# Optimization experiments

Hardware: AMD Instinct MI355X
Metric: run time of the kernel (lower is better)

Reference implementation:

```python
import jax, jax.numpy as jnp
import numpy as np

B, S, HID, NH, HD, NL = 2, 4096, 1024, 16, 64, 128
N_ITER = 6


def setup_inputs() -> dict:
    key = jax.random.key(0)
    ks = jax.random.split(key, 9)
    s = 0.02
    D = NH * HD
    return {
        "X": jax.random.normal(ks[0], (B, S, HID), jnp.float32),
        "mask": jnp.ones((B, S), jnp.float32),
        "Wq": jax.random.normal(ks[1], (HID, D), jnp.float32) * s,
        "bq": jnp.zeros((D,), jnp.float32),
        "Wk": jax.random.normal(ks[2], (HID, D), jnp.float32) * s,
        "bk": jnp.zeros((D,), jnp.float32),
        "Wv": jax.random.normal(ks[3], (HID, D), jnp.float32) * s,
        "bv": jnp.zeros((D,), jnp.float32),
        "Wo": jax.random.normal(ks[4], (D, HID), jnp.float32) * s,
        "bo": jnp.zeros((HID,), jnp.float32),
    }


def iterative_inv(mat, n_iter=N_ITER):
    # Newton-Schulz style pseudo-inverse iteration (Nystromformer 'original' init)
    I = jnp.eye(mat.shape[-1], dtype=mat.dtype)
    K = mat
    V = K.swapaxes(-1, -2) / jnp.max(jnp.sum(K, axis=-2))
    for _ in range(n_iter):
        KV = K @ V
        V = 0.25 * V @ (13.0 * I - KV @ (15.0 * I - KV @ (7.0 * I - KV)))
    return V


def nystrom_core(Q, K, V, mask):
    # Q,K,V: [B,NH,S,HD], mask: [B,S]
    scale = 1.0 / np.sqrt(np.sqrt(HD))  # 1/d^(1/4) applied to both Q and K
    m = mask[:, None, :, None]
    Q = Q * m * scale
    K = K * m * scale
    seg = S // NL
    # landmarks: mean over contiguous segments -> [B,NH,NL,HD]
    Ql = Q.reshape(B, NH, NL, seg, HD).mean(axis=-2)
    Kl = K.reshape(B, NH, NL, seg, HD).mean(axis=-2)
    k1 = jax.nn.softmax(jnp.einsum('bhsd,bhld->bhsl', Q, Kl), axis=-1)   # [B,NH,S,NL]
    k2 = jax.nn.softmax(jnp.einsum('bhld,bhmd->bhlm', Ql, Kl), axis=-1)  # [B,NH,NL,NL]
    k3 = jax.nn.softmax(
        jnp.einsum('bhld,bhsd->bhls', Ql, K) - 1e9 * (1.0 - mask[:, None, None, :]),
        axis=-1)                                                          # [B,NH,NL,S]
    return k1 @ iterative_inv(k2) @ (k3 @ V)                              # [B,NH,S,HD]


def reference(X, mask, Wq, bq, Wk, bk, Wv, bv, Wo, bo):
    def split(Y):  # [B,S,NH*HD] -> [B,NH,S,HD]
        return Y.reshape(B, S, NH, HD).transpose(0, 2, 1, 3)
    Q = split(X @ Wq + bq)
    K = split(X @ Wk + bk)
    V = split(X @ Wv + bv)
    attn = nystrom_core(Q.astype(jnp.float32), K.astype(jnp.float32),
                        V.astype(jnp.float32), mask.astype(jnp.float32))
    out = attn.transpose(0, 2, 1, 3).reshape(B, S, NH * HD)
    return out @ Wo + bo
```

## Files before the change

kernel.cpp:

```cpp
#include <hip/hip_runtime.h>
#include <math.h>

constexpr int cB = 2, cS = 4096, cHID = 1024, cNH = 16, cHD = 64, cNL = 128, cSEG = 32, cD = 1024, cBH = 32;
constexpr float cSCALE = 0.35355339059327373f;

typedef _Float16 f16x8 __attribute__((ext_vector_type(8)));
typedef float f32x4 __attribute__((ext_vector_type(4)));

__device__ inline void gload_lds16(const void* g, void* l) {
    __builtin_amdgcn_global_load_lds(
        (const __attribute__((address_space(1))) void*)g,
        (__attribute__((address_space(3))) void*)l, 16, 0, 0);
}

__global__ __launch_bounds__(256) void wcast_t(
    const float* __restrict__ Wq, const float* __restrict__ Wk,
    const float* __restrict__ Wv, const float* __restrict__ Wo,
    _Float16* __restrict__ WqT, _Float16* __restrict__ WkT,
    _Float16* __restrict__ WvT, _Float16* __restrict__ WoT)
{
    __shared__ float tile[32][33];
    const int wsel = blockIdx.z;
    const float* W = (wsel == 0) ? Wq : (wsel == 1 ? Wk : (wsel == 2 ? Wv : Wo));
    _Float16* WT   = (wsel == 0) ? WqT : (wsel == 1 ? WkT : (wsel == 2 ? WvT : WoT));
    const int n0 = blockIdx.x * 32, k0 = blockIdx.y * 32;
    const int t = threadIdx.x;
    const int r = t >> 3, c = (t & 7) * 4;
    float4 v = *reinterpret_cast<const float4*>(W + (size_t)(k0 + r) * cD + n0 + c);
    tile[r][c] = v.x; tile[r][c + 1] = v.y; tile[r][c + 2] = v.z; tile[r][c + 3] = v.w;
    __syncthreads();
    union { _Float16 h[4]; ushort4 u; } p;
    p.h[0] = (_Float16)tile[c + 0][r]; p.h[1] = (_Float16)tile[c + 1][r];
    p.h[2] = (_Float16)tile[c + 2][r]; p.h[3] = (_Float16)tile[c + 3][r];
    *reinterpret_cast<ushort4*>(WT + (size_t)(n0 + r) * cHID + k0 + c) = p.u;
}

__global__ __launch_bounds__(256) void xm_kernel(
    const float* __restrict__ X, const float* __restrict__ mask,
    float* __restrict__ Xm, float* __restrict__ mbar, _Float16* __restrict__ Xh)
{
    const int bl = blockIdx.x;
    const int b = bl >> 7, l = bl & 127;
    const int c = threadIdx.x * 4;
    float4 a = {0.f, 0.f, 0.f, 0.f};
    float msum = 0.f;
    for (int j = 0; j < cSEG; ++j) {
        float m = mask[b * cS + l * cSEG + j];
        size_t roff = ((size_t)(b * cS + l * cSEG + j)) * cHID + c;
        float4 x = *reinterpret_cast<const float4*>(X + roff);
        union { _Float16 h[4]; ushort4 u; } p;
        p.h[0] = (_Float16)x.x; p.h[1] = (_Float16)x.y;
        p.h[2] = (_Float16)x.z; p.h[3] = (_Float16)x.w;
        *reinterpret_cast<ushort4*>(Xh + roff) = p.u;
        a.x += m * x.x; a.y += m * x.y; a.z += m * x.z; a.w += m * x.w;
        msum += m;
    }
    const float inv = 1.0f / cSEG;
    a.x *= inv; a.y *= inv; a.z *= inv; a.w *= inv;
    *reinterpret_cast<float4*>(Xm + (size_t)bl * cHID + c) = a;
    if (threadIdx.x == 0) mbar[bl] = msum * inv;
}

__global__ __launch_bounds__(256) void qkv_gemm_f16(
    const _Float16* __restrict__ Xh, const float* __restrict__ mask,
    const _Float16* __restrict__ WqT, const _Float16* __restrict__ WkT, const _Float16* __restrict__ WvT,
    const float* __restrict__ bq, const float* __restrict__ bk, const float* __restrict__ bv,
    _Float16* __restrict__ Qh, _Float16* __restrict__ Kh, _Float16* __restrict__ Vh)
{
    __shared__ __align__(16) _Float16 As[128 * 64];
    __shared__ __align__(16) _Float16 Bs[128 * 64];
    const int wsel = blockIdx.z;
    const _Float16* WT = (wsel == 0) ? WqT : (wsel == 1 ? WkT : WvT);
    const float* bias  = (wsel == 0) ? bq  : (wsel == 1 ? bk  : bv);
    _Float16* Y        = (wsel == 0) ? Qh  : (wsel == 1 ? Kh  : Vh);
    const int orig = blockIdx.x;
    const int xcd = orig & 7, idx = orig >> 3;
    const int n0 = (idx & 7) * 128;
    const int m0 = (xcd * 8 + (idx >> 3)) * 128;
    const int t = threadIdx.x;
    const int wave = t >> 6, lane = t & 63;
    const int wm = (wave >> 1) * 64, wn = (wave & 1) * 64;
    const int quad = lane >> 4, l15 = lane & 15;
    const int srow = wave * 8 + (lane >> 3);
    const int scol = ((lane & 7) ^ (lane >> 3)) * 8;

    f32x4 acc[4][4];
#pragma unroll
    for (int i = 0; i < 4; ++i)
#pragma unroll
        for (int j = 0; j < 4; ++j) acc[i][j] = (f32x4){0.f, 0.f, 0.f, 0.f};

    for (int k0 = 0; k0 < cHID; k0 += 64) {
        const _Float16* aSrc = Xh + (size_t)(m0 + srow) * cHID + k0 + scol;
// ... 216 lines not shown
        for (int mt_ = 0; mt_ < 4; ++mt_) {                                             \
            const int rowL_ = wr * 64 + mt_ * 16 + l15;                                 \
            _Pragma("unroll")                                                           \
            for (int k0_ = 0; k0_ < 4; ++k0_) {                                         \
                LH[mt_][k0_] = *reinterpret_cast<const f16x8*>(&PH[rowL_ * 136 + k0_ * 32 + quad * 8]); \
                LL[mt_][k0_] = *reinterpret_cast<const f16x8*>(&PL[rowL_ * 136 + k0_ * 32 + quad * 8]); \
            }                                                                           \
        }                                                                               \
    }

#define NYS_PRODUCT(PH, PL, LH, LL)                                                     \
    {                                                                                   \
        _Pragma("unroll")                                                               \
        for (int mt_ = 0; mt_ < 4; ++mt_)                                               \
            _Pragma("unroll")                                                           \
            for (int nt_ = 0; nt_ < 2; ++nt_) acc[mt_][nt_] = (f32x4){0.f, 0.f, 0.f, 0.f}; \
        _Pragma("unroll")                                                               \
        for (int nt_ = 0; nt_ < 2; ++nt_) {                                             \
            _Pragma("unroll")                                                           \
            for (int k0_ = 0; k0_ < 4; ++k0_) {                                         \
                const int boff_ = (wcb + nt_ * 16) * 136 + k0_ * 32 + quad * 8;         \
                f16x8 bh_ = *reinterpret_cast<const f16x8*>(&PH[boff_]);                \
                f16x8 bl_ = *reinterpret_cast<const f16x8*>(&PL[boff_]);                \
                _Pragma("unroll")                                                       \
                for (int mt_ = 0; mt_ < 4; ++mt_) {                                     \
                    acc[mt_][nt_] = NYS_MFMA(LH[mt_][k0_], bh_, acc[mt_][nt_]);         \
                    acc[mt_][nt_] = NYS_MFMA(LL[mt_][k0_], bh_, acc[mt_][nt_]);         \
                    acc[mt_][nt_] = NYS_MFMA(LH[mt_][k0_], bl_, acc[mt_][nt_]);         \
                }                                                                       \
            }                                                                           \
        }                                                                               \
    }

__global__ __launch_bounds__(512, 2) void nys_fused(
    const float* __restrict__ k2, const int* __restrict__ cmax,
    float* __restrict__ Mg0, float* __restrict__ Mg1)
{
    __shared__ __align__(16) _Float16 Ahi_s[128 * 136];
    __shared__ __align__(16) _Float16 Alo_s[128 * 136];
    __shared__ __align__(16) _Float16 Whi_s[128 * 136];
    __shared__ __align__(16) _Float16 Wlo_s[128 * 136];
    const int bh = blockIdx.x;
    const int t = threadIdx.x;
    const int wave = t >> 6, lane = t & 63;
    const int wr = wave >> 2, wc = wave & 3;
    const int quad = lane >> 4, l15 = lane & 15;
    const int wcb = wc * 32 + l15;
    const float* Kg = k2 + (size_t)bh * 16384;
    float* Mg0b = Mg0 + (size_t)bh * 16384;
    float* Mg1b = Mg1 + (size_t)bh * 16384;
    const float sc = sqrtf(1.0f / __int_as_float(*cmax));

    {
        const int row = t >> 2, c0 = (t & 3) * 32;
        const float* src = Kg + row * 128 + c0;
        _Float16* dh = &Whi_s[row * 136 + c0];
        _Float16* dl = &Wlo_s[row * 136 + c0];
#pragma unroll
        for (int u = 0; u < 32; u += 4) {
            float4 v = *reinterpret_cast<const float4*>(src + u);
            ushort4 ph, pl; _Float16 h, l;
            split2(v.x * sc, h, l); ph.x = f16bits(h); pl.x = f16bits(l);
            split2(v.y * sc, h, l); ph.y = f16bits(h); pl.y = f16bits(l);
            split2(v.z * sc, h, l); ph.z = f16bits(h); pl.z = f16bits(l);
            split2(v.w * sc, h, l); ph.w = f16bits(h); pl.w = f16bits(l);
            *reinterpret_cast<ushort4*>(dh + u) = ph;
            *reinterpret_cast<ushort4*>(dl + u) = pl;
        }
    }
    __syncthreads();

    f32x4 acc[4][2];
    f16x8 Fh[4][4], Fl[4][4];

    NYS_PRELOAD(Whi_s, Wlo_s, Fh, Fl);
    NYS_PRODUCT(Whi_s, Wlo_s, Fh, Fl);
#pragma unroll
    for (int mt = 0; mt < 4; ++mt)
#pragma unroll
        for (int nt = 0; nt < 2; ++nt) {
            const int col = wcb + nt * 16;
            const int rb  = wr * 64 + mt * 16 + quad * 4;
            ushort4 ph, pl;
#pragma unroll
            for (int r = 0; r < 4; ++r) {
                _Float16 h, l; split2(acc[mt][nt][r], h, l);
                ((unsigned short*)&ph)[r] = f16bits(h);
                ((unsigned short*)&pl)[r] = f16bits(l);
            }
            *reinterpret_cast<ushort4*>(&Ahi_s[col * 136 + rb]) = ph;
            *reinterpret_cast<ushort4*>(&Alo_s[col * 136 + rb]) = pl;
        }
    __syncthreads();

    for (int it = 0; it < 6; ++it) {
        NYS_PRELOAD(Ahi_s, Alo_s, Fh, Fl);
        NYS_PRODUCT(Ahi_s, Alo_s, Fh, Fl);
#pragma unroll
        for (int mt = 0; mt < 4; ++mt)
#pragma unroll
            for (int nt = 0; nt < 2; ++nt) {
                const int col = wcb + nt * 16;
                const int rb  = wr * 64 + mt * 16 + quad * 4;
                ushort4 ah = *reinterpret_cast<const ushort4*>(&Ahi_s[col * 136 + rb]);
                ushort4 al = *reinterpret_cast<const ushort4*>(&Alo_s[col * 136 + rb]);
                ushort4 ph, pl;
#pragma unroll
                for (int r = 0; r < 4; ++r) {
                    float av = (float)__builtin_bit_cast(_Float16, ((unsigned short*)&ah)[r])
                             + (float)__builtin_bit_cast(_Float16, ((unsigned short*)&al)[r]);
                    float v = ((rb + r) == col ? 15.0f : 0.0f) - 7.0f * av + acc[mt][nt][r];
                    _Float16 h, l; split2(v, h, l);
                    ((unsigned short*)&ph)[r] = f16bits(h);
                    ((unsigned short*)&pl)[r] = f16bits(l);
                }
                *reinterpret_cast<ushort4*>(&Whi_s[col * 136 + rb]) = ph;
                *reinterpret_cast<ushort4*>(&Wlo_s[col * 136 + rb]) = pl;
            }
        __syncthreads();
        NYS_PRODUCT(Whi_s, Wlo_s, Fh, Fl);
        __syncthreads();
#pragma unroll
        for (int mt = 0; mt < 4; ++mt)
#pragma unroll
            for (int nt = 0; nt < 2; ++nt) {
                const int col = wcb + nt * 16;
                const int rb  = wr * 64 + mt * 16 + quad * 4;
                ushort4 ph, pl; float4 mv;
#pragma unroll
                for (int r = 0; r < 4; ++r) {
                    float v = ((rb + r) == col ? 13.0f : 0.0f) - acc[mt][nt][r];
                    _Float16 h, l; split2(v, h, l);
                    ((unsigned short*)&ph)[r] = f16bits(h);
                    ((unsigned short*)&pl)[r] = f16bits(l);
                    ((float*)&mv)[r] = 0.25f * v;
                }
                *reinterpret_cast<ushort4*>(&Whi_s[col * 136 + rb]) = ph;
                *reinterpret_cast<ushort4*>(&Wlo_s[col * 136 + rb]) = pl;
                if (it == 0)
                    *reinterpret_cast<float4*>(&Mg0b[col * 128 + rb]) = mv;
            }
        __syncthreads();
        NYS_PRODUCT(Whi_s, Wlo_s, Fh, Fl);
#pragma unroll
        for (int mt = 0; mt < 4; ++mt)
#pragma unroll
            for (int nt = 0; nt < 2; ++nt) {
                const int col = wcb + nt * 16;
                const int rb  = wr * 64 + mt * 16 + quad * 4;
                ushort4 ph, pl;
#pragma unroll
                for (int r = 0; r < 4; ++r) {
                    _Float16 h, l; split2(0.25f * acc[mt][nt][r], h, l);
                    ((unsigned short*)&ph)[r] = f16bits(h);
                    ((unsigned short*)&pl)[r] = f16bits(l);
                }
                *reinterpret_cast<ushort4*>(&Ahi_s[col * 136 + rb]) = ph;
                *reinterpret_cast<ushort4*>(&Alo_s[col * 136 + rb]) = pl;
            }
        if (it >= 1) {
            const float* Mr = (it & 1) ? Mg0b : Mg1b;
            float*       Mw = (it & 1) ? Mg1b : Mg0b;
#pragma unroll
            for (int mt = 0; mt < 4; ++mt)
#pragma unroll
                for (int nt = 0; nt < 2; ++nt) acc[mt][nt] = (f32x4){0.f, 0.f, 0.f, 0.f};
#pragma unroll
            for (int k0 = 0; k0 < 4; ++k0) {
                f16x8 Mh[4], Ml[4];
#pragma unroll
                for (int mt = 0; mt < 4; ++mt) {
                    const int rowL = wr * 64 + mt * 16 + l15;
                    const float* src = Mr + rowL * 128 + k0 * 32 + quad * 8;
                    float4 v0 = *reinterpret_cast<const float4*>(src);
                    float4 v1 = *reinterpret_cast<const float4*>(src + 4);
                    union { f16x8 v; _Float16 e[8]; } hh, ll;
                    split2(v0.x, hh.e[0], ll.e[0]); split2(v0.y, hh.e[1], ll.e[1]);
                    split2(v0.z, hh.e[2], ll.e[2]); split2(v0.w, hh.e[3], ll.e[3]);
                    split2(v1.x, hh.e[4], ll.e[4]); split2(v1.y, hh.e[5], ll.e[5]);
                    split2(v1.z, hh.e[6], ll.e[6]); split2(v1.w, hh.e[7], ll.e[7]);
                    Mh[mt] = hh.v; Ml[mt] = ll.v;
                }
#pragma unroll
                for (int nt = 0; nt < 2; ++nt) {
                    const int boff = (wcb + nt * 16) * 136 + k0 * 32 + quad * 8;
                    f16x8 bh_ = *reinterpret_cast<const f16x8*>(&Whi_s[boff]);
                    f16x8 bl_ = *reinterpret_cast<const f16x8*>(&Wlo_s[boff]);
#pragma unroll
                    for (int mt = 0; mt < 4; ++mt) {
                        acc[mt][nt] = NYS_MFMA(Mh[mt], bh_, acc[mt][nt]);
                        acc[mt][nt] = NYS_MFMA(Ml[mt], bh_, acc[mt][nt]);
                        acc[mt][nt] = NYS_MFMA(Mh[mt], bl_, acc[mt][nt]);
                    }
                }
            }
#pragma unroll
            for (int mt = 0; mt < 4; ++mt)
#pragma unroll
                for (int nt = 0; nt < 2; ++nt) {
                    const int col = wcb + nt * 16;
                    const int rb  = wr * 64 + mt * 16 + quad * 4;
                    float4 mv;
#pragma unroll
                    for (int r = 0; r < 4; ++r) ((float*)&mv)[r] = 0.25f * acc[mt][nt][r];
                    *reinterpret_cast<float4*>(&Mw[col * 128 + rb]) = mv;
                }
        }
        __syncthreads();
    }
}

__global__ __launch_bounds__(256) void vtrans(const _Float16* __restrict__ Vh, _Float16* __restrict__ VTh)
{
    __shared__ ushort T[64][72];
    const int s0 = blockIdx.x * 64, bh = blockIdx.y;
    const int t = threadIdx.x;
    const _Float16* vb = Vh + ((size_t)bh * cS + s0) * cHD;
#pragma unroll
    for (int i = 0; i < 2; ++i) {
        int idx = t + i * 256;
        int row = idx >> 3, c8 = idx & 7;
        f16x8 v = *reinterpret_cast<const f16x8*>(vb + (size_t)row * cHD + c8 * 8);
#pragma unroll
        for (int j = 0; j < 8; ++j) T[row][c8 * 8 + j] = ((ushort*)&v)[j];
    }
    __syncthreads();
    _Float16* vt = VTh + (size_t)bh * cHD * cS;
#pragma unroll
    for (int i = 0; i < 2; ++i) {
        int idx = t + i * 256;
        int d = idx >> 3, s8 = idx & 7;
        f16x8 o;
#pragma unroll
        for (int j = 0; j < 8; ++j) ((ushort*)&o)[j] = T[s8 * 8 + j][d];
        *reinterpret_cast<f16x8*>(vt + (size_t)d * cS + s0 + s8 * 8) = o;
    }
}

__global__ __launch_bounds__(256) void k3v_mfma(
    const _Float16* __restrict__ Qlh, const _Float16* __restrict__ Kh,
    const _Float16* __restrict__ VTh, const float* __restrict__ mask,
    float* __restrict__ Opart, float* __restrict__ mpart, float* __restrict__ spart)
{
    __shared__ __align__(16) _Float16 Ps[128 * 72];
    __shared__ float msk[256];
    const int z = blockIdx.x, bh = blockIdx.y;
    const int b = bh >> 4;
    const int sbase = z * 256;
    const int t = threadIdx.x;
    const int wave = t >> 6, lane = t & 63;
    const int quad = lane >> 4, l15 = lane & 15;

    msk[t] = mask[b * cS + sbase + t];

    f16x8 aq[2][2];
    const _Float16* qlg = Qlh + (size_t)bh * cNL * cHD;
#pragma unroll
    for (int mt = 0; mt < 2; ++mt)
#pragma unroll
        for (int k0 = 0; k0 < 2; ++k0)
            aq[mt][k0] = *reinterpret_cast<const f16x8*>(
                qlg + (size_t)(wave * 32 + mt * 16 + l15) * cHD + k0 * 32 + quad * 8);

    float mrun[2][4], srun[2][4];
    f32x4 accO[2][4];
#pragma unroll
    for (int mt = 0; mt < 2; ++mt)
#pragma unroll
        for (int r = 0; r < 4; ++r) { mrun[mt][r] = -1e30f; srun[mt][r] = 0.f; }
#pragma unroll
    for (int mt = 0; mt < 2; ++mt)
#pragma unroll
        for (int dt = 0; dt < 4; ++dt) accO[mt][dt] = (f32x4){0.f, 0.f, 0.f, 0.f};

    __syncthreads();

    const _Float16* kg = Kh + (size_t)bh * cS * cHD;
    const _Float16* vg = VTh + (size_t)bh * cHD * cS;

    for (int step = 0; step < 4; ++step) {
        const int st = sbase + step * 64;
        f32x4 accS[2][4];
#pragma unroll
        for (int mt = 0; mt < 2; ++mt)
#pragma unroll
            for (int nt = 0; nt < 4; ++nt) accS[mt][nt] = (f32x4){0.f, 0.f, 0.f, 0.f};
#pragma unroll
        for (int k0 = 0; k0 < 2; ++k0)
#pragma unroll
            for (int nt = 0; nt < 4; ++nt) {
                f16x8 bk = *reinterpret_cast<const f16x8*>(
                    kg + (size_t)(st + nt * 16 + l15) * cHD + k0 * 32 + quad * 8);
#pragma unroll
                for (int mt = 0; mt < 2; ++mt)
                    accS[mt][nt] = __builtin_amdgcn_mfma_f32_16x16x32_f16(aq[mt][k0], bk, accS[mt][nt], 0, 0, 0);
            }
#pragma unroll
        for (int nt = 0; nt < 4; ++nt) {
            float pen = 1e9f * (1.0f - msk[step * 64 + nt * 16 + l15]);
#pragma unroll
            for (int mt = 0; mt < 2; ++mt)
#pragma unroll
                for (int r = 0; r < 4; ++r) accS[mt][nt][r] -= pen;
        }
#pragma unroll
        for (int mt = 0; mt < 2; ++mt) {
#pragma unroll
            for (int r = 0; r < 4; ++r) {
                float tmax = fmaxf(fmaxf(accS[mt][0][r], accS[mt][1][r]),
                                   fmaxf(accS[mt][2][r], accS[mt][3][r]));
#pragma unroll
                for (int w = 1; w < 16; w <<= 1) tmax = fmaxf(tmax, __shfl_xor(tmax, w, 16));
                float mnew = fmaxf(mrun[mt][r], tmax);
                float alpha = __expf(mrun[mt][r] - mnew);
                float ts = 0.f;
#pragma unroll
                for (int nt = 0; nt < 4; ++nt) {
                    float e = __expf(accS[mt][nt][r] - mnew);
                    accS[mt][nt][r] = e; ts += e;
                }
#pragma unroll
                for (int w = 1; w < 16; w <<= 1) ts += __shfl_xor(ts, w, 16);
                srun[mt][r] = srun[mt][r] * alpha + ts;
                mrun[mt][r] = mnew;
#pragma unroll
                for (int dt = 0; dt < 4; ++dt) accO[mt][dt][r] *= alpha;
            }
        }
#pragma unroll
        for (int mt = 0; mt < 2; ++mt)
#pragma unroll
            for (int nt = 0; nt < 4; ++nt)
#pragma unroll
                for (int r = 0; r < 4; ++r)
                    Ps[(wave * 32 + mt * 16 + quad * 4 + r) * 72 + nt * 16 + l15] =
                        (_Float16)accS[mt][nt][r];
#pragma unroll
        for (int k0 = 0; k0 < 2; ++k0) {
            f16x8 ap[2];
#pragma unroll
            for (int mt = 0; mt < 2; ++mt)
                ap[mt] = *reinterpret_cast<const f16x8*>(
                    &Ps[(wave * 32 + mt * 16 + l15) * 72 + k0 * 32 + quad * 8]);
#pragma unroll
            for (int dt = 0; dt < 4; ++dt) {
                f16x8 bv = *reinterpret_cast<const f16x8*>(
                    vg + (size_t)(dt * 16 + l15) * cS + st + k0 * 32 + quad * 8);
#pragma unroll
                for (int mt = 0; mt < 2; ++mt)
                    accO[mt][dt] = __builtin_amdgcn_mfma_f32_16x16x32_f16(ap[mt], bv, accO[mt][dt], 0, 0, 0);
            }
        }
    }
    const int rowbase = bh * cNL + wave * 32;
#pragma unroll
    for (int mt = 0; mt < 2; ++mt)
#pragma unroll
        for (int dt = 0; dt < 4; ++dt)
#pragma unroll
            for (int r = 0; r < 4; ++r)
                Opart[(size_t)(z * 4096 + rowbase + mt * 16 + quad * 4 + r) * cHD + dt * 16 + l15] =
                    accO[mt][dt][r];
    if (l15 == 0) {
#pragma unroll
        for (int mt = 0; mt < 2; ++mt)
#pragma unroll
            for (int r = 0; r < 4; ++r) {
                int prow = z * 4096 + rowbase + mt * 16 + quad * 4 + r;
                mpart[prow] = mrun[mt][r];
                spart[prow] = srun[mt][r];
            }
    }
}

__global__ __launch_bounds__(256) void k3v_reduce(
    const float* __restrict__ Opart, const float* __restrict__ mpart,
    const float* __restrict__ spart, float* __restrict__ CV)
{
    const int t = threadIdx.x;
    const int row = blockIdx.x * 4 + (t >> 6);
    const int d = t & 63;
    float mstar = -1e30f;
#pragma unroll
    for (int z = 0; z < 16; ++z) mstar = fmaxf(mstar, mpart[z * 4096 + row]);
    float ssum = 0.f, acc = 0.f;
#pragma unroll
    for (int z = 0; z < 16; ++z) {
        float w = __expf(mpart[z * 4096 + row] - mstar);
        ssum += w * spart[z * 4096 + row];
        acc  += w * Opart[(size_t)(z * 4096 + row) * cHD + d];
    }
    CV[(size_t)row * cHD + d] = acc / ssum;
}

__global__ __launch_bounds__(256) void w2_matmul(
    const float* __restrict__ k2, const float* __restrict__ M6,
    const int* __restrict__ cmax, const float* __restrict__ CV,
    _Float16* __restrict__ W2T)
{
    __shared__ __align__(16) float CVs[128][68];
    __shared__ __align__(16) float Us[128][68];
    const int bh = blockIdx.x, t = threadIdx.x;
    const float invc = 1.0f / __int_as_float(*cmax);
    for (int k = 0; k < 32; ++k) { int idx = t + k * 256; CVs[idx >> 6][idx & 63] = CV[(size_t)bh * 8192 + idx]; }
    __syncthreads();
    const float* Mg = M6 + (size_t)bh * 16384;
    {
        const int tx = t & 15, ty = t >> 4;
        float acc[8][4] = {};
        for (int k = 0; k < 128; ++k) {
            float4 b4 = *reinterpret_cast<const float4*>(&CVs[k][tx * 4]);
#pragma unroll
            for (int i = 0; i < 8; ++i) {
                float a = Mg[(ty * 8 + i) * 128 + k];
                acc[i][0] += a * b4.x; acc[i][1] += a * b4.y; acc[i][2] += a * b4.z; acc[i][3] += a * b4.w;
            }
        }
#pragma unroll
        for (int i = 0; i < 8; ++i)
#pragma unroll
            for (int j = 0; j < 4; ++j)
                Us[ty * 8 + i][tx * 4 + j] = acc[i][j];
    }
    __syncthreads();
    {
        const int l = t & 127, dg = (t >> 7) * 32;
        float acc2[32];
#pragma unroll
        for (int dd = 0; dd < 32; ++dd) acc2[dd] = 0.f;
        const float* kg = k2 + (size_t)bh * 16384;
        for (int j = 0; j < 128; ++j) {
            float kv = kg[j * 128 + l];
#pragma unroll
            for (int dd = 0; dd < 32; ++dd) acc2[dd] += kv * Us[j][dg + dd];
        }
        _Float16* wt = W2T + (size_t)bh * (cHD * cNL);
#pragma unroll
// ... 96 lines not shown
{
    const float* X    = (const float*)d_in[0];
    const float* mask = (const float*)d_in[1];
    const float* Wq   = (const float*)d_in[2];
    const float* bq   = (const float*)d_in[3];
    const float* Wk   = (const float*)d_in[4];
    const float* bk   = (const float*)d_in[5];
    const float* Wv   = (const float*)d_in[6];
    const float* bv   = (const float*)d_in[7];
    const float* Wo   = (const float*)d_in[8];
    const float* bo   = (const float*)d_in[9];
    float* out = (float*)d_out;

    float* ws = (float*)d_ws;
    size_t off = 0;
    const size_t szQKV = (size_t)cBH * cS * cHD;
    const size_t szL   = (size_t)cBH * cNL * cHD;
    const size_t szM   = (size_t)cBH * cNL * cNL;
    float* Qr   = ws + off; off += szQKV;
    float* Kr   = ws + off; off += szQKV;
    float* Vr   = ws + off; off += szQKV;
    _Float16* Xh  = (_Float16*)(ws + off); off += szQKV / 2;
    _Float16* WqT = (_Float16*)(ws + off); off += 524288;
    _Float16* WkT = (_Float16*)(ws + off); off += 524288;
    _Float16* WvT = (_Float16*)(ws + off); off += 524288;
    _Float16* WoT = (_Float16*)(ws + off); off += 524288;
    float* Xm   = ws + off; off += (size_t)cB * cNL * cHID;
    float* mbar = ws + off; off += 256;
    float* Ql  = ws + off; off += szL;
    float* Kl  = ws + off; off += szL;
    float* k2  = ws + off; off += szM;
    float* Mg0 = ws + off; off += szM;
    float* Mg1 = ws + off; off += szM;
    float* Zb  = ws + off; off += szM;
    float* T2b = ws + off; off += szM;
    float* T3b = ws + off; off += szM;
    float* CV  = ws + off; off += szL;
    _Float16* Qlh  = (_Float16*)(ws + off); off += szL / 2;
    _Float16* Klh  = (_Float16*)(ws + off); off += szL / 2;
    _Float16* W2Th = (_Float16*)(ws + off); off += szL / 2;
    int*   cmax = (int*)(ws + off); off += 16;
    float* mpart = ws + off; off += 65536;
    float* spart = ws + off; off += 65536;

    _Float16* Qh   = (_Float16*)Qr;
    float*    Opart = Qr + szQKV / 2;
    _Float16* Kh   = (_Float16*)Kr;
    _Float16* ctxh = (_Float16*)(Kr + szQKV / 2);
    _Float16* Vh   = (_Float16*)Vr;
    _Float16* VTh  = (_Float16*)(Vr + szQKV / 2);

    (void)Zb; (void)T2b; (void)T3b;

    hipMemsetAsync(cmax, 0, sizeof(int), stream);

    wcast_t<<<dim3(32, 32, 4), 256, 0, stream>>>(Wq, Wk, Wv, Wo, WqT, WkT, WvT, WoT);
    xm_kernel<<<cB * cNL, 256, 0, stream>>>(X, mask, Xm, mbar, Xh);

    qkv_gemm_f16<<<dim3(512, 1, 3), 256, 0, stream>>>(
        Xh, mask, WqT, WkT, WvT, bq, bk, bv, Qh, Kh, Vh);
    vtrans<<<dim3(cS / 64, cBH), 256, 0, stream>>>(Vh, VTh);
    lgemm<<<dim3(cD / 64, (cB * cNL) / 64, 2), 256, 0, stream>>>(Xm, mbar, Wq, bq, Wk, bk, Ql, Kl, Qlh, Klh);

    k2_softmax<<<cBH * cNL, 128, 0, stream>>>(Ql, Kl, k2);
    colsum_max<<<cBH, 128, 0, stream>>>(k2, cmax);

    nys_fused<<<cBH, 512, 0, stream>>>(k2, cmax, Mg0, Mg1);

    k3v_mfma<<<dim3(16, cBH), 256, 0, stream>>>(Qlh, Kh, VTh, mask, Opart, mpart, spart);
    k3v_reduce<<<1024, 256, 0, stream>>>(Opart, mpart, spart, CV);
    w2_matmul<<<cBH, 256, 0, stream>>>(k2, Mg1, cmax, CV, W2Th);
    k1_mfma<<<dim3(cS / 64, cBH), 256, 0, stream>>>(Qh, Klh, W2Th, ctxh);
    out_gemm_f16<<<dim3(512), 256, 0, stream>>>(ctxh, WoT, bo, out);
}
```

Measured before the change: 474.2 us.

## Co-schedule Newton-Schulz inverse with k3·V in one launch, fold reduce into w2

The 32-block serial Newton-Schulz inverse kernel and the k3·V flash-style partial kernel now run as a single launch. The first 32 blocks do the inverse and the remaining 256 blocks each run two k3v work-groups of 4 waves, so the two independent stages overlap on the GPU. The k3v_reduce kernel is removed and its log-sum-exp combine is done inside w2_matmul when it loads CV. xm_kernel is split across 4 blocks of 64 threads per segment to raise parallelism. The cost is that the heterogeneous blocks share one large LDS allocation sized for the inverse path, which may limit occupancy for the k3v blocks, and w2_matmul now repeats redundant reduction work.

Measured after the change: 476.5 us. About the same (+0.5%).

```diff
diff --git a/kernel.cpp b/kernel.cpp
--- a/kernel.cpp
+++ b/kernel.cpp
@@ -35,13 +35,14 @@
     *reinterpret_cast<ushort4*>(WT + (size_t)(n0 + r) * cHID + k0 + c) = p.u;
 }
 
-__global__ __launch_bounds__(256) void xm_kernel(
+__global__ __launch_bounds__(64) void xm_kernel(
     const float* __restrict__ X, const float* __restrict__ mask,
     float* __restrict__ Xm, float* __restrict__ mbar, _Float16* __restrict__ Xh)
 {
     const int bl = blockIdx.x;
+    const int q  = blockIdx.y;
     const int b = bl >> 7, l = bl & 127;
-    const int c = threadIdx.x * 4;
+    const int c = q * 256 + threadIdx.x * 4;
     float4 a = {0.f, 0.f, 0.f, 0.f};
     float msum = 0.f;
     for (int j = 0; j < cSEG; ++j) {
@@ -58,7 +59,7 @@
     const float inv = 1.0f / cSEG;
     a.x *= inv; a.y *= inv; a.z *= inv; a.w *= inv;
     *reinterpret_cast<float4*>(Xm + (size_t)bl * cHID + c) = a;
-    if (threadIdx.x == 0) mbar[bl] = msum * inv;
+    if (q == 0 && threadIdx.x == 0) mbar[bl] = msum * inv;
 }
 
 __global__ __launch_bounds__(256) void qkv_gemm_f16(
@@ -341,115 +342,54 @@
         }                                                                               \
     }
 
-__global__ __launch_bounds__(512, 2) void nys_fused(
+__global__ __launch_bounds__(512, 2) void nys_k3v(
     const float* __restrict__ k2, const int* __restrict__ cmax,
-    float* __restrict__ Mg0, float* __restrict__ Mg1)
-{
-    __shared__ __align__(16) _Float16 Ahi_s[128 * 136];
-    __shared__ __align__(16) _Float16 Alo_s[128 * 136];
-    __shared__ __align__(16) _Float16 Whi_s[128 * 136];
-    __shared__ __align__(16) _Float16 Wlo_s[128 * 136];
-    const int bh = blockIdx.x;
-    const int t = threadIdx.x;
-    const int wave = t >> 6, lane = t & 63;
-    const int wr = wave >> 2, wc = wave & 3;
-    const int quad = lane >> 4, l15 = lane & 15;
-    const int wcb = wc * 32 + l15;
-    const float* Kg = k2 + (size_t)bh * 16384;
-    float* Mg0b = Mg0 + (size_t)bh * 16384;
-    float* Mg1b = Mg1 + (size_t)bh * 16384;
-    const float sc = sqrtf(1.0f / __int_as_float(*cmax));
-
-    {
-        const int row = t >> 2, c0 = (t & 3) * 32;
-        const float* src = Kg + row * 128 + c0;
-        _Float16* dh = &Whi_s[row * 136 + c0];
-        _Float16* dl = &Wlo_s[row * 136 + c0];
-#pragma unroll
-        for (int u = 0; u < 32; u += 4) {
-            float4 v = *reinterpret_cast<const float4*>(src + u);
-            ushort4 ph, pl; _Float16 h, l;
-            split2(v.x * sc, h, l); ph.x = f16bits(h); pl.x = f16bits(l);
-            split2(v.y * sc, h, l); ph.y = f16bits(h); pl.y = f16bits(l);
-            split2(v.z * sc, h, l); ph.z = f16bits(h); pl.z = f16bits(l);
-            split2(v.w * sc, h, l); ph.w = f16bits(h); pl.w = f16bits(l);
-            *reinterpret_cast<ushort4*>(dh + u) = ph;
-            *reinterpret_cast<ushort4*>(dl + u) = pl;
-        }
-    }
-    __syncthreads();
-
-    f32x4 acc[4][2];
-    f16x8 Fh[4][4], Fl[4][4];
-
-    NYS_PRELOAD(Whi_s, Wlo_s, Fh, Fl);
-    NYS_PRODUCT(Whi_s, Wlo_s, Fh, Fl);
-#pragma unroll
-    for (int mt = 0; mt < 4; ++mt)
-#pragma unroll
-        for (int nt = 0; nt < 2; ++nt) {
-            const int col = wcb + nt * 16;
-            const int rb  = wr * 64 + mt * 16 + quad * 4;
-            ushort4 ph, pl;
-#pragma unroll
-            for (int r = 0; r < 4; ++r) {
-                _Float16 h, l; split2(acc[mt][nt][r], h, l);
-                ((unsigned short*)&ph)[r] = f16bits(h);
-                ((unsigned short*)&pl)[r] = f16bits(l);
+    float* __restrict__ Mg0, float* __restrict__ Mg1,
+    const _Float16* __restrict__ Qlh, const _Float16* __restrict__ Kh,
+    const _Float16* __restrict__ VTh, const float* __restrict__ mask,
+    float* __restrict__ Opart, float* __restrict__ mpart, float* __restrict__ spart)
+{
+    __shared__ __align__(16) _Float16 SMEM[4 * 128 * 136];
+
+    if (blockIdx.x < 32) {
+        _Float16* Ahi_s = SMEM;
+        _Float16* Alo_s = SMEM + 128 * 136;
+        _Float16* Whi_s = SMEM + 2 * 128 * 136;
+        _Float16* Wlo_s = SMEM + 3 * 128 * 136;
+        const int bh = blockIdx.x;
+        const int t = threadIdx.x;
+        const int wave = t >> 6, lane = t & 63;
+        const int wr = wave >> 2, wc = wave & 3;
+        const int quad = lane >> 4, l15 = lane & 15;
+        const int wcb = wc * 32 + l15;
+        const float* Kg = k2 + (size_t)bh * 16384;
+        float* Mg0b = Mg0 + (size_t)bh * 16384;
+        float* Mg1b = Mg1 + (size_t)bh * 16384;
+        const float sc = sqrtf(1.0f / __int_as_float(*cmax));
+
+        {
+            const int row = t >> 2, c0 = (t & 3) * 32;
+            const float* src = Kg + row * 128 + c0;
+            _Float16* dh = &Whi_s[row * 136 + c0];
+            _Float16* dl = &Wlo_s[row * 136 + c0];
+#pragma unroll
+            for (int u = 0; u < 32; u += 4) {
+                float4 v = *reinterpret_cast<const float4*>(src + u);
+                ushort4 ph, pl; _Float16 h, l;
+                split2(v.x * sc, h, l); ph.x = f16bits(h); pl.x = f16bits(l);
+                split2(v.y * sc, h, l); ph.y = f16bits(h); pl.y = f16bits(l);
+                split2(v.z * sc, h, l); ph.z = f16bits(h); pl.z = f16bits(l);
+                split2(v.w * sc, h, l); ph.w = f16bits(h); pl.w = f16bits(l);
+                *reinterpret_cast<ushort4*>(dh + u) = ph;
+                *reinterpret_cast<ushort4*>(dl + u) = pl;
             }
-            *reinterpret_cast<ushort4*>(&Ahi_s[col * 136 + rb]) = ph;
-            *reinterpret_cast<ushort4*>(&Alo_s[col * 136 + rb]) = pl;
-        }
-    __syncthreads();
-
-    for (int it = 0; it < 6; ++it) {
-        NYS_PRELOAD(Ahi_s, Alo_s, Fh, Fl);
-        NYS_PRODUCT(Ahi_s, Alo_s, Fh, Fl);
-#pragma unroll
-        for (int mt = 0; mt < 4; ++mt)
-#pragma unroll
-            for (int nt = 0; nt < 2; ++nt) {
-                const int col = wcb + nt * 16;
-                const int rb  = wr * 64 + mt * 16 + quad * 4;
-                ushort4 ah = *reinterpret_cast<const ushort4*>(&Ahi_s[col * 136 + rb]);
-                ushort4 al = *reinterpret_cast<const ushort4*>(&Alo_s[col * 136 + rb]);
-                ushort4 ph, pl;
-#pragma unroll
-                for (int r = 0; r < 4; ++r) {
-                    float av = (float)__builtin_bit_cast(_Float16, ((unsigned short*)&ah)[r])
-                             + (float)__builtin_bit_cast(_Float16, ((unsigned short*)&al)[r]);
-                    float v = ((rb + r) == col ? 15.0f : 0.0f) - 7.0f * av + acc[mt][nt][r];
-                    _Float16 h, l; split2(v, h, l);
-                    ((unsigned short*)&ph)[r] = f16bits(h);
-                    ((unsigned short*)&pl)[r] = f16bits(l);
-                }
-                *reinterpret_cast<ushort4*>(&Whi_s[col * 136 + rb]) = ph;
-                *reinterpret_cast<ushort4*>(&Wlo_s[col * 136 + rb]) = pl;
-            }
+        }
         __syncthreads();
-        NYS_PRODUCT(Whi_s, Wlo_s, Fh, Fl);
-        __syncthreads();
-#pragma unroll
-        for (int mt = 0; mt < 4; ++mt)
-#pragma unroll
-            for (int nt = 0; nt < 2; ++nt) {
-                const int col = wcb + nt * 16;
-                const int rb  = wr * 64 + mt * 16 + quad * 4;
-                ushort4 ph, pl; float4 mv;
-#pragma unroll
-                for (int r = 0; r < 4; ++r) {
-                    float v = ((rb + r) == col ? 13.0f : 0.0f) - acc[mt][nt][r];
-                    _Float16 h, l; split2(v, h, l);
-                    ((unsigned short*)&ph)[r] = f16bits(h);
-                    ((unsigned short*)&pl)[r] = f16bits(l);
-                    ((float*)&mv)[r] = 0.25f * v;
-                }
-                *reinterpret_cast<ushort4*>(&Whi_s[col * 136 + rb]) = ph;
-                *reinterpret_cast<ushort4*>(&Wlo_s[col * 136 + rb]) = pl;
-                if (it == 0)
-                    *reinterpret_cast<float4*>(&Mg0b[col * 128 + rb]) = mv;
-            }
-        __syncthreads();
+
+        f32x4 acc[4][2];
+        f16x8 Fh[4][4], Fl[4][4];
+
+        NYS_PRELOAD(Whi_s, Wlo_s, Fh, Fl);
         NYS_PRODUCT(Whi_s, Wlo_s, Fh, Fl);
 #pragma unroll
         for (int mt = 0; mt < 4; ++mt)
@@ -460,62 +400,259 @@
                 ushort4 ph, pl;
 #pragma unroll
                 for (int r = 0; r < 4; ++r) {
-                    _Float16 h, l; split2(0.25f * acc[mt][nt][r], h, l);
+                    _Float16 h, l; split2(acc[mt][nt][r], h, l);
                     ((unsigned short*)&ph)[r] = f16bits(h);
                     ((unsigned short*)&pl)[r] = f16bits(l);
                 }
                 *reinterpret_cast<ushort4*>(&Ahi_s[col * 136 + rb]) = ph;
                 *reinterpret_cast<ushort4*>(&Alo_s[col * 136 + rb]) = pl;
             }
-        if (it >= 1) {
-            const float* Mr = (it & 1) ? Mg0b : Mg1b;
-            float*       Mw = (it & 1) ? Mg1b : Mg0b;
-#pragma unroll
-            for (int mt = 0; mt < 4; ++mt)
-#pragma unroll
-                for (int nt = 0; nt < 2; ++nt) acc[mt][nt] = (f32x4){0.f, 0.f, 0.f, 0.f};
-#pragma unroll
-            for (int k0 = 0; k0 < 4; ++k0) {
-                f16x8 Mh[4], Ml[4];
-#pragma unroll
-                for (int mt = 0; mt < 4; ++mt) {
-                    const int rowL = wr * 64 + mt * 16 + l15;
-                    const float* src = Mr + rowL * 128 + k0 * 32 + quad * 8;
-                    float4 v0 = *reinterpret_cast<const float4*>(src);
-                    float4 v1 = *reinterpret_cast<const float4*>(src + 4);
-                    union { f16x8 v; _Float16 e[8]; } hh, ll;
-                    split2(v0.x, hh.e[0], ll.e[0]); split2(v0.y, hh.e[1], ll.e[1]);
-                    split2(v0.z, hh.e[2], ll.e[2]); split2(v0.w, hh.e[3], ll.e[3]);
-                    split2(v1.x, hh.e[4], ll.e[4]); split2(v1.y, hh.e[5], ll.e[5]);
-                    split2(v1.z, hh.e[6], ll.e[6]); split2(v1.w, hh.e[7], ll.e[7]);
-                    Mh[mt] = hh.v; Ml[mt] = ll.v;
-                }
-#pragma unroll
-                for (int nt = 0; nt < 2; ++nt) {
-                    const int boff = (wcb + nt * 16) * 136 + k0 * 32 + quad * 8;
-                    f16x8 bh_ = *reinterpret_cast<const f16x8*>(&Whi_s[boff]);
-                    f16x8 bl_ = *reinterpret_cast<const f16x8*>(&Wlo_s[boff]);
-#pragma unroll
-                    for (int mt = 0; mt < 4; ++mt) {
-                        acc[mt][nt] = NYS_MFMA(Mh[mt], bh_, acc[mt][nt]);
-                        acc[mt][nt] = NYS_MFMA(Ml[mt], bh_, acc[mt][nt]);
-                        acc[mt][nt] = NYS_MFMA(Mh[mt], bl_, acc[mt][nt]);
-                    }
-                }
-            }
+        __syncthreads();
+
+        for (int it = 0; it < 6; ++it) {
+            NYS_PRELOAD(Ahi_s, Alo_s, Fh, Fl);
+            NYS_PRODUCT(Ahi_s, Alo_s, Fh, Fl);
 #pragma unroll
             for (int mt = 0; mt < 4; ++mt)
 #pragma unroll
                 for (int nt = 0; nt < 2; ++nt) {
                     const int col = wcb + nt * 16;
                     const int rb  = wr * 64 + mt * 16 + quad * 4;
-                    float4 mv;
-#pragma unroll
-                    for (int r = 0; r < 4; ++r) ((float*)&mv)[r] = 0.25f * acc[mt][nt][r];
-                    *reinterpret_cast<float4*>(&Mw[col * 128 + rb]) = mv;
+                    ushort4 ah = *reinterpret_cast<const ushort4*>(&Ahi_s[col * 136 + rb]);
+                    ushort4 al = *reinterpret_cast<const ushort4*>(&Alo_s[col * 136 + rb]);
+                    ushort4 ph, pl;
+#pragma unroll
+                    for (int r = 0; r < 4; ++r) {
+                        float av = (float)__builtin_bit_cast(_Float16, ((unsigned short*)&ah)[r])
+                                 + (float)__builtin_bit_cast(_Float16, ((unsigned short*)&al)[r]);
+                        float v = ((rb + r) == col ? 15.0f : 0.0f) - 7.0f * av + acc[mt][nt][r];
+                        _Float16 h, l; split2(v, h, l);
+                        ((unsigned short*)&ph)[r] = f16bits(h);
+                        ((unsigned short*)&pl)[r] = f16bits(l);
+                    }
+                    *reinterpret_cast<ushort4*>(&Whi_s[col * 136 + rb]) = ph;
+                    *reinterpret_cast<ushort4*>(&Wlo_s[col * 136 + rb]) = pl;
                 }
-        }
-        __syncthreads();
+            __syncthreads();
+            NYS_PRODUCT(Whi_s, Wlo_s, Fh, Fl);
+            __syncthreads();
+#pragma unroll
+            for (int mt = 0; mt < 4; ++mt)
+#pragma unroll
+                for (int nt = 0; nt < 2; ++nt) {
+                    const int col = wcb + nt * 16;
+                    const int rb  = wr * 64 + mt * 16 + quad * 4;
+                    ushort4 ph, pl; float4 mv;
+#pragma unroll
+                    for (int r = 0; r < 4; ++r) {
+                        float v = ((rb + r) == col ? 13.0f : 0.0f) - acc[mt][nt][r];
+                        _Float16 h, l; split2(v, h, l);
+                        ((unsigned short*)&ph)[r] = f16bits(h);
+                        ((unsigned short*)&pl)[r] = f16bits(l);
+                        ((float*)&mv)[r] = 0.25f * v;
+                    }
+                    *reinterpret_cast<ushort4*>(&Whi_s[col * 136 + rb]) = ph;
+                    *reinterpret_cast<ushort4*>(&Wlo_s[col * 136 + rb]) = pl;
+                    if (it == 0)
+                        *reinterpret_cast<float4*>(&Mg0b[col * 128 + rb]) = mv;
+                }
+            __syncthreads();
+            NYS_PRODUCT(Whi_s, Wlo_s, Fh, Fl);
+#pragma unroll
+            for (int mt = 0; mt < 4; ++mt)
+#pragma unroll
+                for (int nt = 0; nt < 2; ++nt) {
+                    const int col = wcb + nt * 16;
+                    const int rb  = wr * 64 + mt * 16 + quad * 4;
+                    ushort4 ph, pl;
+#pragma unroll
+                    for (int r = 0; r < 4; ++r) {
+                        _Float16 h, l; split2(0.25f * acc[mt][nt][r], h, l);
+                        ((unsigned short*)&ph)[r] = f16bits(h);
+                        ((unsigned short*)&pl)[r] = f16bits(l);
+                    }
+                    *reinterpret_cast<ushort4*>(&Ahi_s[col * 136 + rb]) = ph;
+                    *reinterpret_cast<ushort4*>(&Alo_s[col * 136 + rb]) = pl;
+                }
+            if (it >= 1) {
+                const float* Mr = (it & 1) ? Mg0b : Mg1b;
+                float*       Mw = (it & 1) ? Mg1b : Mg0b;
+#pragma unroll
+                for (int mt = 0; mt < 4; ++mt)
+#pragma unroll
+                    for (int nt = 0; nt < 2; ++nt) acc[mt][nt] = (f32x4){0.f, 0.f, 0.f, 0.f};
+#pragma unroll
+                for (int k0 = 0; k0 < 4; ++k0) {
+                    f16x8 Mh[4], Ml[4];
+#pragma unroll
+                    for (int mt = 0; mt < 4; ++mt) {
+                        const int rowL = wr * 64 + mt * 16 + l15;
+                        const float* src = Mr + rowL * 128 + k0 * 32 + quad * 8;
+                        float4 v0 = *reinterpret_cast<const float4*>(src);
+                        float4 v1 = *reinterpret_cast<const float4*>(src + 4);
+                        union { f16x8 v; _Float16 e[8]; } hh, ll;
+                        split2(v0.x, hh.e[0], ll.e[0]); split2(v0.y, hh.e[1], ll.e[1]);
+                        split2(v0.z, hh.e[2], ll.e[2]); split2(v0.w, hh.e[3], ll.e[3]);
+                        split2(v1.x, hh.e[4], ll.e[4]); split2(v1.y, hh.e[5], ll.e[5]);
+                        split2(v1.z, hh.e[6], ll.e[6]); split2(v1.w, hh.e[7], ll.e[7]);
+                        Mh[mt] = hh.v; Ml[mt] = ll.v;
+                    }
+#pragma unroll
+                    for (int nt = 0; nt < 2; ++nt) {
+                        const int boff = (wcb + nt * 16) * 136 + k0 * 32 + quad * 8;
+                        f16x8 bh_ = *reinterpret_cast<const f16x8*>(&Whi_s[boff]);
+                        f16x8 bl_ = *reinterpret_cast<const f16x8*>(&Wlo_s[boff]);
+#pragma unroll
+                        for (int mt = 0; mt < 4; ++mt) {
+                            acc[mt][nt] = NYS_MFMA(Mh[mt], bh_, acc[mt][nt]);
+                            acc[mt][nt] = NYS_MFMA(Ml[mt], bh_, acc[mt][nt]);
+                            acc[mt][nt] = NYS_MFMA(Mh[mt], bl_, acc[mt][nt]);
+                        }
+                    }
+                }
+#pragma unroll
+                for (int mt = 0; mt < 4; ++mt)
+#pragma unroll
+                    for (int nt = 0; nt < 2; ++nt) {
+                        const int col = wcb + nt * 16;
+                        const int rb  = wr * 64 + mt * 16 + quad * 4;
+                        float4 mv;
+#pragma unroll
+                        for (int r = 0; r < 4; ++r) ((float*)&mv)[r] = 0.25f * acc[mt][nt][r];
+                        *reinterpret_cast<float4*>(&Mw[col * 128 + rb]) = mv;
+                    }
+            }
+            __syncthreads();
+        }
+    } else {
+        const int t = threadIdx.x;
+        const int wave8 = t >> 6;
+        const int wg = wave8 >> 2;
+        const int wave = wave8 & 3;
+        _Float16* Ps = SMEM + (size_t)wg * (128 * 72);
+        const int zz = (blockIdx.x - 32) * 2 + wg;
+        const int z = zz & 15, bh = zz >> 4;
+        const int b = bh >> 4;
+        const int sbase = z * 256;
+        const int lane = t & 63;
+        const int quad = lane >> 4, l15 = lane & 15;
+
+        f16x8 aq[2][2];
+        const _Float16* qlg = Qlh + (size_t)bh * cNL * cHD;
+#pragma unroll
+        for (int mt = 0; mt < 2; ++mt)
+#pragma unroll
+            for (int k0 = 0; k0 < 2; ++k0)
+                aq[mt][k0] = *reinterpret_cast<const f16x8*>(
+                    qlg + (size_t)(wave * 32 + mt * 16 + l15) * cHD + k0 * 32 + quad * 8);
+
+        float mrun[2][4], srun[2][4];
+        f32x4 accO[2][4];
+#pragma unroll
+        for (int mt = 0; mt < 2; ++mt)
+#pragma unroll
+            for (int r = 0; r < 4; ++r) { mrun[mt][r] = -1e30f; srun[mt][r] = 0.f; }
+#pragma unroll
+        for (int mt = 0; mt < 2; ++mt)
+#pragma unroll
+            for (int dt = 0; dt < 4; ++dt) accO[mt][dt] = (f32x4){0.f, 0.f, 0.f, 0.f};
+
+        const _Float16* kg = Kh + (size_t)bh * cS * cHD;
+        const _Float16* vg = VTh + (size_t)bh * cHD * cS;
+
+        for (int step = 0; step < 4; ++step) {
+            const int st = sbase + step * 64;
+            f32x4 accS[2][4];
+#pragma unroll
+            for (int mt = 0; mt < 2; ++mt)
+#pragma unroll
+                for (int nt = 0; nt < 4; ++nt) accS[mt][nt] = (f32x4){0.f, 0.f, 0.f, 0.f};
+#pragma unroll
+            for (int k0 = 0; k0 < 2; ++k0)
+#pragma unroll
+                for (int nt = 0; nt < 4; ++nt) {
+                    f16x8 bk = *reinterpret_cast<const f16x8*>(
+                        kg + (size_t)(st + nt * 16 + l15) * cHD + k0 * 32 + quad * 8);
+#pragma unroll
+                    for (int mt = 0; mt < 2; ++mt)
+                        accS[mt][nt] = __builtin_amdgcn_mfma_f32_16x16x32_f16(aq[mt][k0], bk, accS[mt][nt], 0, 0, 0);
+                }
+#pragma unroll
+            for (int nt = 0; nt < 4; ++nt) {
+                float pen = 1e9f * (1.0f - mask[b * cS + st + nt * 16 + l15]);
+#pragma unroll
+                for (int mt = 0; mt < 2; ++mt)
+#pragma unroll
+                    for (int r = 0; r < 4; ++r) accS[mt][nt][r] -= pen;
+            }
+#pragma unroll
+            for (int mt = 0; mt < 2; ++mt) {
+#pragma unroll
+                for (int r = 0; r < 4; ++r) {
+                    float tmax = fmaxf(fmaxf(accS[mt][0][r], accS[mt][1][r]),
+                                       fmaxf(accS[mt][2][r], accS[mt][3][r]));
+#pragma unroll
+                    for (int w = 1; w < 16; w <<= 1) tmax = fmaxf(tmax, __shfl_xor(tmax, w, 16));
+                    float mnew = fmaxf(mrun[mt][r], tmax);
+                    float alpha = __expf(mrun[mt][r] - mnew);
+                    float ts = 0.f;
+#pragma unroll
+                    for (int nt = 0; nt < 4; ++nt) {
+                        float e = __expf(accS[mt][nt][r] - mnew);
+                        accS[mt][nt][r] = e; ts += e;
+                    }
+#pragma unroll
+                    for (int w = 1; w < 16; w <<= 1) ts += __shfl_xor(ts, w, 16);
+                    srun[mt][r] = srun[mt][r] * alpha + ts;
+                    mrun[mt][r] = mnew;
+#pragma unroll
+                    for (int dt = 0; dt < 4; ++dt) accO[mt][dt][r] *= alpha;
+                }
+            }
+#pragma unroll
+            for (int mt = 0; mt < 2; ++mt)
+#pragma unroll
+                for (int nt = 0; nt < 4; ++nt)
+#pragma unroll
+                    for (int r = 0; r < 4; ++r)
+                        Ps[(wave * 32 + mt * 16 + quad * 4 + r) * 72 + nt * 16 + l15] =
+                            (_Float16)accS[mt][nt][r];
+#pragma unroll
+            for (int k0 = 0; k0 < 2; ++k0) {
+                f16x8 ap[2];
+#pragma unroll
+                for (int mt = 0; mt < 2; ++mt)
+                    ap[mt] = *reinterpret_cast<const f16x8*>(
+                        &Ps[(wave * 32 + mt * 16 + l15) * 72 + k0 * 32 + quad * 8]);
+#pragma unroll
+                for (int dt = 0; dt < 4; ++dt) {
+                    f16x8 bv = *reinterpret_cast<const f16x8*>(
+                        vg + (size_t)(dt * 16 + l15) * cS + st + k0 * 32 + quad * 8);
+#pragma unroll
+                    for (int mt = 0; mt < 2; ++mt)
+                        accO[mt][dt] = __builtin_amdgcn_mfma_f32_16x16x32_f16(ap[mt], bv, accO[mt][dt], 0, 0, 0);
+                }
+            }
+        }
+        const int rowbase = bh * cNL + wave * 32;
+#pragma unroll
+        for (int mt = 0; mt < 2; ++mt)
+#pragma unroll
+            for (int dt = 0; dt < 4; ++dt)
+#pragma unroll
+                for (int r = 0; r < 4; ++r)
+                    Opart[(size_t)(z * 4096 + rowbase + mt * 16 + quad * 4 + r) * cHD + dt * 16 + l15] =
+                        accO[mt][dt][r];
+        if (l15 == 0) {
+#pragma unroll
+            for (int mt = 0; mt < 2; ++mt)
+#pragma unroll
+                for (int r = 0; r < 4; ++r) {
+                    int prow = z * 4096 + rowbase + mt * 16 + quad * 4 + r;
+                    mpart[prow] = mrun[mt][r];
+                    spart[prow] = srun[mt][r];
+                }
+        }
     }
 }
 
@@ -546,172 +683,33 @@
     }
 }
 
-__global__ __launch_bounds__(256) void k3v_mfma(
-    const _Float16* __restrict__ Qlh, const _Float16* __restrict__ Kh,
-    const _Float16* __restrict__ VTh, const float* __restrict__ mask,
-    float* __restrict__ Opart, float* __restrict__ mpart, float* __restrict__ spart)
-{
-    __shared__ __align__(16) _Float16 Ps[128 * 72];
-    __shared__ float msk[256];
-    const int z = blockIdx.x, bh = blockIdx.y;
-    const int b = bh >> 4;
-    const int sbase = z * 256;
-    const int t = threadIdx.x;
-    const int wave = t >> 6, lane = t & 63;
-    const int quad = lane >> 4, l15 = lane & 15;
-
-    msk[t] = mask[b * cS + sbase + t];
-
-    f16x8 aq[2][2];
-    const _Float16* qlg = Qlh + (size_t)bh * cNL * cHD;
-#pragma unroll
-    for (int mt = 0; mt < 2; ++mt)
-#pragma unroll
-        for (int k0 = 0; k0 < 2; ++k0)
-            aq[mt][k0] = *reinterpret_cast<const f16x8*>(
-                qlg + (size_t)(wave * 32 + mt * 16 + l15) * cHD + k0 * 32 + quad * 8);
-
-    float mrun[2][4], srun[2][4];
-    f32x4 accO[2][4];
-#pragma unroll
-    for (int mt = 0; mt < 2; ++mt)
-#pragma unroll
-        for (int r = 0; r < 4; ++r) { mrun[mt][r] = -1e30f; srun[mt][r] = 0.f; }
-#pragma unroll
-    for (int mt = 0; mt < 2; ++mt)
-#pragma unroll
-        for (int dt = 0; dt < 4; ++dt) accO[mt][dt] = (f32x4){0.f, 0.f, 0.f, 0.f};
-
-    __syncthreads();
-
-    const _Float16* kg = Kh + (size_t)bh * cS * cHD;
-    const _Float16* vg = VTh + (size_t)bh * cHD * cS;
-
-    for (int step = 0; step < 4; ++step) {
-        const int st = sbase + step * 64;
-        f32x4 accS[2][4];
-#pragma unroll
-        for (int mt = 0; mt < 2; ++mt)
-#pragma unroll
-            for (int nt = 0; nt < 4; ++nt) accS[mt][nt] = (f32x4){0.f, 0.f, 0.f, 0.f};
-#pragma unroll
-        for (int k0 = 0; k0 < 2; ++k0)
-#pragma unroll
-            for (int nt = 0; nt < 4; ++nt) {
-                f16x8 bk = *reinterpret_cast<const f16x8*>(
-                    kg + (size_t)(st + nt * 16 + l15) * cHD + k0 * 32 + quad * 8);
-#pragma unroll
-                for (int mt = 0; mt < 2; ++mt)
-                    accS[mt][nt] = __builtin_amdgcn_mfma_f32_16x16x32_f16(aq[mt][k0], bk, accS[mt][nt], 0, 0, 0);
-            }
-#pragma unroll
-        for (int nt = 0; nt < 4; ++nt) {
-            float pen = 1e9f * (1.0f - msk[step * 64 + nt * 16 + l15]);
-#pragma unroll
-            for (int mt = 0; mt < 2; ++mt)
-#pragma unroll
-                for (int r = 0; r < 4; ++r) accS[mt][nt][r] -= pen;
-        }
-#pragma unroll
-        for (int mt = 0; mt < 2; ++mt) {
-#pragma unroll
-            for (int r = 0; r < 4; ++r) {
-                float tmax = fmaxf(fmaxf(accS[mt][0][r], accS[mt][1][r]),
-                                   fmaxf(accS[mt][2][r], accS[mt][3][r]));
-#pragma unroll
-                for (int w = 1; w < 16; w <<= 1) tmax = fmaxf(tmax, __shfl_xor(tmax, w, 16));
-                float mnew = fmaxf(mrun[mt][r], tmax);
-                float alpha = __expf(mrun[mt][r] - mnew);
-                float ts = 0.f;
-#pragma unroll
-                for (int nt = 0; nt < 4; ++nt) {
-                    float e = __expf(accS[mt][nt][r] - mnew);
-                    accS[mt][nt][r] = e; ts += e;
-                }
-#pragma unroll
-                for (int w = 1; w < 16; w <<= 1) ts += __shfl_xor(ts, w, 16);
-                srun[mt][r] = srun[mt][r] * alpha + ts;
-                mrun[mt][r] = mnew;
-#pragma unroll
-                for (int dt = 0; dt < 4; ++dt) accO[mt][dt][r] *= alpha;
-            }
-        }
-#pragma unroll
-        for (int mt = 0; mt < 2; ++mt)
-#pragma unroll
-            for (int nt = 0; nt < 4; ++nt)
-#pragma unroll
-                for (int r = 0; r < 4; ++r)
-                    Ps[(wave * 32 + mt * 16 + quad * 4 + r) * 72 + nt * 16 + l15] =
-                        (_Float16)accS[mt][nt][r];
-#pragma unroll
-        for (int k0 = 0; k0 < 2; ++k0) {
-            f16x8 ap[2];
-#pragma unroll
-            for (int mt = 0; mt < 2; ++mt)
-                ap[mt] = *reinterpret_cast<const f16x8*>(
-                    &Ps[(wave * 32 + mt * 16 + l15) * 72 + k0 * 32 + quad * 8]);
-#pragma unroll
-            for (int dt = 0; dt < 4; ++dt) {
-                f16x8 bv = *reinterpret_cast<const f16x8*>(
-                    vg + (size_t)(dt * 16 + l15) * cS + st + k0 * 32 + quad * 8);
-#pragma unroll
-                for (int mt = 0; mt < 2; ++mt)
-                    accO[mt][dt] = __builtin_amdgcn_mfma_f32_16x16x32_f16(ap[mt], bv, accO[mt][dt], 0, 0, 0);
-            }
-        }
-    }
-    const int rowbase = bh * cNL + wave * 32;
-#pragma unroll
-    for (int mt = 0; mt < 2; ++mt)
-#pragma unroll
-        for (int dt = 0; dt < 4; ++dt)
-#pragma unroll
-            for (int r = 0; r < 4; ++r)
-                Opart[(size_t)(z * 4096 + rowbase + mt * 16 + quad * 4 + r) * cHD + dt * 16 + l15] =
-                    accO[mt][dt][r];
-    if (l15 == 0) {
-#pragma unroll
-        for (int mt = 0; mt < 2; ++mt)
-#pragma unroll
-            for (int r = 0; r < 4; ++r) {
-                int prow = z * 4096 + rowbase + mt * 16 + quad * 4 + r;
-                mpart[prow] = mrun[mt][r];
-                spart[prow] = srun[mt][r];
-            }
-    }
-}
-
-__global__ __launch_bounds__(256) void k3v_reduce(
-    const float* __restrict__ Opart, const float* __restrict__ mpart,
-    const float* __restrict__ spart, float* __restrict__ CV)
-{
-    const int t = threadIdx.x;
-    const int row = blockIdx.x * 4 + (t >> 6);
-    const int d = t & 63;
-    float mstar = -1e30f;
-#pragma unroll
-    for (int z = 0; z < 16; ++z) mstar = fmaxf(mstar, mpart[z * 4096 + row]);
-    float ssum = 0.f, acc = 0.f;
-#pragma unroll
-    for (int z = 0; z < 16; ++z) {
-        float w = __expf(mpart[z * 4096 + row] - mstar);
-        ssum += w * spart[z * 4096 + row];
-        acc  += w * Opart[(size_t)(z * 4096 + row) * cHD + d];
-    }
-    CV[(size_t)row * cHD + d] = acc / ssum;
-}
-
 __global__ __launch_bounds__(256) void w2_matmul(
     const float* __restrict__ k2, const float* __restrict__ M6,
-    const int* __restrict__ cmax, const float* __restrict__ CV,
+    const int* __restrict__ cmax,
+    const float* __restrict__ Opart, const float* __restrict__ mpart,
+    const float* __restrict__ spart,
     _Float16* __restrict__ W2T)
 {
     __shared__ __align__(16) float CVs[128][68];
     __shared__ __align__(16) float Us[128][68];
     const int bh = blockIdx.x, t = threadIdx.x;
     const float invc = 1.0f / __int_as_float(*cmax);
-    for (int k = 0; k < 32; ++k) { int idx = t + k * 256; CVs[idx >> 6][idx & 63] = CV[(size_t)bh * 8192 + idx]; }
+    for (int it = 0; it < 32; ++it) {
+        int idx = t + it * 256;
+        int row = idx >> 6, d = idx & 63;
+        int grow = bh * cNL + row;
+        float mstar = -1e30f;
+#pragma unroll
+        for (int z = 0; z < 16; ++z) mstar = fmaxf(mstar, mpart[z * 4096 + grow]);
+        float ssum = 0.f, acc = 0.f;
+#pragma unroll
+        for (int z = 0; z < 16; ++z) {
+            float w = __expf(mpart[z * 4096 + grow] - mstar);
+            ssum += w * spart[z * 4096 + grow];
+            acc  += w * Opart[(size_t)(z * 4096 + grow) * cHD + d];
+        }
+        CVs[row][d] = acc / ssum;
+    }
     __syncthreads();
     const float* Mg = M6 + (size_t)bh * 16384;
     {
@@ -874,7 +872,7 @@
     float* k2  = ws + off; off += szM;
     float* Mg0 = ws + off; off += szM;
     float* Mg1 = ws + off; off += szM;
-    float* Zb  = ws + off; off += szM;
+    float* T1b = ws + off; off += szM;
     float* T2b = ws + off; off += szM;
     float* T3b = ws + off; off += szM;
     float* CV  = ws + off; off += szL;
@@ -892,12 +890,12 @@
     _Float16* Vh   = (_Float16*)Vr;
     _Float16* VTh  = (_Float16*)(Vr + szQKV / 2);
 
-    (void)Zb; (void)T2b; (void)T3b;
+    (void)T1b; (void)T2b; (void)T3b; (void)CV;
 
     hipMemsetAsync(cmax, 0, sizeof(int), stream);
 
     wcast_t<<<dim3(32, 32, 4), 256, 0, stream>>>(Wq, Wk, Wv, Wo, WqT, WkT, WvT, WoT);
-    xm_kernel<<<cB * cNL, 256, 0, stream>>>(X, mask, Xm, mbar, Xh);
+    xm_kernel<<<dim3(cB * cNL, 4), 64, 0, stream>>>(X, mask, Xm, mbar, Xh);
 
     qkv_gemm_f16<<<dim3(512, 1, 3), 256, 0, stream>>>(
         Xh, mask, WqT, WkT, WvT, bq, bk, bv, Qh, Kh, Vh);
@@ -907,11 +905,10 @@
     k2_softmax<<<cBH * cNL, 128, 0, stream>>>(Ql, Kl, k2);
     colsum_max<<<cBH, 128, 0, stream>>>(k2, cmax);
 
-    nys_fused<<<cBH, 512, 0, stream>>>(k2, cmax, Mg0, Mg1);
-
-    k3v_mfma<<<dim3(16, cBH), 256, 0, stream>>>(Qlh, Kh, VTh, mask, Opart, mpart, spart);
-    k3v_reduce<<<1024, 256, 0, stream>>>(Opart, mpart, spart, CV);
-    w2_matmul<<<cBH, 256, 0, stream>>>(k2, Mg1, cmax, CV, W2Th);
+    nys_k3v<<<dim3(32 + 256), 512, 0, stream>>>(
+        k2, cmax, Mg0, Mg1, Qlh, Kh, VTh, mask, Opart, mpart, spart);
+
+    w2_matmul<<<cBH, 256, 0, stream>>>(k2, Mg1, cmax, Opart, mpart, spart, W2Th);
     k1_mfma<<<dim3(cS / 64, cBH), 256, 0, stream>>>(Qh, Klh, W2Th, ctxh);
     out_gemm_f16<<<dim3(512), 256, 0, stream>>>(ctxh, WoT, bo, out);
 }
```
